# Kernel optimization log

Measured on AMD Instinct MI355X. Metric: run time of the kernel, lower is better.

## Reference

```python
import jax, jax.numpy as jnp
import numpy as np

TOP_K = 2


def setup_inputs() -> dict:
    key = jax.random.key(0)
    k1, k2, k3, k4, k5 = jax.random.split(key, 5)
    H, F, E = 1024, 2048, 8
    B, S = 2, 1024
    return {
        "hidden_states": jax.random.normal(k1, (B, S, H), dtype=jnp.float32),
        "gate_w": jax.random.normal(k2, (E, H), dtype=jnp.float32) * (1.0 / np.sqrt(H)),
        "w1": jax.random.normal(k3, (E, F, H), dtype=jnp.float32) * (1.0 / np.sqrt(H)),
        "w2": jax.random.normal(k4, (E, H, F), dtype=jnp.float32) * (1.0 / np.sqrt(F)),
        "w3": jax.random.normal(k5, (E, F, H), dtype=jnp.float32) * (1.0 / np.sqrt(H)),
    }


def reference(hidden_states, gate_w, w1, w2, w3):
    B, S, H = hidden_states.shape
    E = gate_w.shape[0]
    x = hidden_states.reshape(-1, H)  # [T, H]

    # Router: softmax in float32, top-k, renormalize (exact Mixtral math)
    router_logits = x @ gate_w.T  # [T, E]
    probs = jax.nn.softmax(router_logits.astype(jnp.float32), axis=-1)
    routing_weights, selected = jax.lax.top_k(probs, TOP_K)  # [T, K]
    routing_weights = routing_weights / routing_weights.sum(axis=-1, keepdims=True)
    routing_weights = routing_weights.astype(x.dtype)

    # Per-token combine weight for each expert: [T, E]
    combine = (jax.nn.one_hot(selected, E, dtype=x.dtype) * routing_weights[..., None]).sum(axis=1)

    # Dense grouped expert SwiGLU MLP (zero combine weight for unselected experts
    # makes this strictly equivalent to the gathered/dispatched computation)
    h = jnp.einsum('th,efh->etf', x, w1)   # [E, T, F]
    g = jnp.einsum('th,efh->etf', x, w3)   # [E, T, F]
    mid = jax.nn.silu(h) * g               # SwiGLU
    expert_out = jnp.einsum('etf,ehf->eth', mid, w2)  # [E, T, H]
    out = jnp.einsum('eth,te->th', expert_out, combine)  # weighted combine

    return out.reshape(B, S, H), router_logits
```

## Files before the change

kernel.cpp:

```cpp
#include <hip/hip_runtime.h>
#include <hip/hip_bf16.h>
#include <math.h>

#define H 1024
#define FF 2048
#define E 8
#define T 2048
#define NSLOT (2*T)
#define SLOT_PAD 128

#define WCONV_BLKS 12288
#define XCONV_BLKS 512
#define ROUTER_BLKS T
#define K1_BLKS (WCONV_BLKS + XCONV_BLKS + ROUTER_BLKS)

typedef __attribute__((ext_vector_type(8))) short s16x8;
typedef __attribute__((ext_vector_type(4))) float f32x4;
typedef __attribute__((ext_vector_type(4))) unsigned int u32x4;

static __device__ __forceinline__ unsigned short f2bf(float f) {
    union { float f; unsigned u; } v; v.f = f;
    unsigned r = v.u + 0x7fff + ((v.u >> 16) & 1);
    return (unsigned short)(r >> 16);
}
static __device__ __forceinline__ float bf2f(unsigned short s) {
    union { unsigned u; float f; } v; v.u = ((unsigned)s) << 16;
    return v.f;
}
static __device__ __forceinline__ unsigned pack2(float a, float b) {
    return (unsigned)f2bf(a) | ((unsigned)f2bf(b) << 16);
}

typedef __attribute__((address_space(3))) unsigned int lds_uint;
typedef const __attribute__((address_space(1))) unsigned int glob_uint;
static __device__ __forceinline__ void gl_lds16(const void* g, void* l) {
    __builtin_amdgcn_global_load_lds((glob_uint*)g, (lds_uint*)l, 16, 0, 0);
}

static __device__ __forceinline__ void expert_range(const int* __restrict__ counts,
                                                    int e, int& off, int& cnt) {
    int acc = 0;
    #pragma unroll
    for (int i = 0; i < E; ++i) {
        int c = counts[i];
        if (i < e) acc += c;
        if (i == e) cnt = c;
    }
    off = acc;
}

__global__ __launch_bounds__(256) void prep_kernel(
    const float* __restrict__ x, const float* __restrict__ gw,
    const float* __restrict__ w1, const float* __restrict__ w3,
    const float* __restrict__ w2,
    unsigned short* __restrict__ w1b, unsigned short* __restrict__ w3b,
    unsigned short* __restrict__ w2b, unsigned short* __restrict__ xb,
    float* __restrict__ logits_out, int* __restrict__ top_id,
    float* __restrict__ top_w, int* __restrict__ counts)
{
    int b = blockIdx.x;
    int tid = threadIdx.x;
    if (b < WCONV_BLKS + XCONV_BLKS) {
        const float* s; unsigned short* d; size_t base;
        if (b < WCONV_BLKS) {
            int r = b >> 12;
            s = (r == 0) ? w1 : (r == 1) ? w3 : w2;
            d = (r == 0) ? w1b : (r == 1) ? w3b : w2b;
            base = (size_t)(b & 4095) * 4096;
        } else {
            s = x; d = xb;
            base = (size_t)(b - WCONV_BLKS) * 4096;
        }
        size_t i0 = base + (size_t)(0 * 256 + tid) * 4;
        size_t i1 = base + (size_t)(1 * 256 + tid) * 4;
        size_t i2 = base + (size_t)(2 * 256 + tid) * 4;
        size_t i3 = base + (size_t)(3 * 256 + tid) * 4;
        f32x4 a0 = __builtin_nontemporal_load((const f32x4*)(s + i0));
        f32x4 a1 = __builtin_nontemporal_load((const f32x4*)(s + i1));
        f32x4 a2 = __builtin_nontemporal_load((const f32x4*)(s + i2));
        f32x4 a3 = __builtin_nontemporal_load((const f32x4*)(s + i3));
        uint2 r0, r1, r2, r3;
        r0.x = pack2(a0.x, a0.y); r0.y = pack2(a0.z, a0.w);
        r1.x = pack2(a1.x, a1.y); r1.y = pack2(a1.z, a1.w);
        r2.x = pack2(a2.x, a2.y); r2.y = pack2(a2.z, a2.w);
        r3.x = pack2(a3.x, a3.y); r3.y = pack2(a3.z, a3.w);
        *(uint2*)(d + i0) = r0;
        *(uint2*)(d + i1) = r1;
        *(uint2*)(d + i2) = r2;
        *(uint2*)(d + i3) = r3;
        return;
    }
    int t = b - (WCONV_BLKS + XCONV_BLKS);
    int e = tid >> 5;
    int l32 = tid & 31;
    const float* xr = x + (size_t)t * H;
    const float* gr = gw + (size_t)e * H;
    float s = 0.f;
    for (int h = l32; h < H; h += 32) s += xr[h] * gr[h];
    for (int off = 16; off; off >>= 1) s += __shfl_down(s, off, 32);
    __shared__ float lg[E];
    if (l32 == 0) lg[e] = s;
    __syncthreads();
    if (tid < E) logits_out[(size_t)t * E + tid] = lg[tid];
    if (tid == 0) {
        int i1 = 0; float b1 = lg[0];
        for (int i = 1; i < E; ++i) if (lg[i] > b1) { b1 = lg[i]; i1 = i; }
        int i2 = -1; float b2 = -INFINITY;
        for (int i = 0; i < E; ++i) if (i != i1 && lg[i] > b2) { b2 = lg[i]; i2 = i; }
        float p2 = expf(b2 - b1);
        float inv = 1.f / (1.f + p2);
        top_id[2*t]   = i1;  top_id[2*t+1] = i2;
        top_w[2*t]    = inv; top_w[2*t+1]  = p2 * inv;
        atomicAdd(&counts[i1], 1);
        atomicAdd(&counts[i2], 1);
    }
}

__global__ __launch_bounds__(256) void assign_kernel(
    const int* __restrict__ top_id, const int* __restrict__ counts,
    int* __restrict__ cursors, int* __restrict__ top_pos,
    int* __restrict__ slot_token)
{
    int t = blockIdx.x * 256 + threadIdx.x;
    if (t >= T) return;
    int offs[E];
    {
        int acc = 0;
        #pragma unroll
        for (int i = 0; i < E; ++i) { offs[i] = acc; acc += counts[i]; }
    }
    #pragma unroll
    for (int k = 0; k < 2; ++k) {
        int e = top_id[2*t + k];
        int p = offs[e] + atomicAdd(&cursors[e], 1);
        top_pos[2*t + k] = p;
        slot_token[p] = t;
    }
}

__global__ __launch_bounds__(256) void gemm1_kernel(
    const unsigned short* __restrict__ xb, const int* __restrict__ slot_token,
    const unsigned short* __restrict__ w1b, const unsigned short* __restrict__ w3b,
    const int* __restrict__ counts, unsigned short* __restrict__ mid)
{
    int e = blockIdx.z;
    int off, cnt;
    expert_range(counts, e, off, cnt);
    int m0 = blockIdx.y * 128;
    if (m0 >= cnt) return;
    int f0 = blockIdx.x * 64;

    __shared__ __align__(16) unsigned short sx[128 * 64];
    __shared__ __align__(16) unsigned short s1[64 * 64];
    __shared__ __align__(16) unsigned short s3[64 * 64];

    int tid = threadIdx.x;
    int wv = tid >> 6, ln = tid & 63;
    int quad = ln >> 4, l16 = ln & 15;
    int wm = wv & 1, wn = wv >> 1;
    int xor7 = l16 & 7;

    const unsigned short* xsrc[4]; unsigned short* xdst[4];
    #pragma unroll
    for (int j = 0; j < 4; ++j) {
        int row = wv * 32 + j * 8 + (ln >> 3);
        int slot = off + m0 + row;
        if (m0 + row >= cnt) slot = off;
        int tok = slot_token[slot];
        int cl = (ln & 7) ^ (row & 7);
        xsrc[j] = xb + (size_t)tok * H + cl * 8;
        xdst[j] = &sx[(wv * 32 + j * 8) * 64];
    }
    const unsigned short *w1s[2], *w3s[2]; unsigned short *d1[2], *d3[2];
    #pragma unroll
    for (int j = 0; j < 2; ++j) {
        int row = wv * 16 + j * 8 + (ln >> 3);
        int cl = (ln & 7) ^ (row & 7);
        w1s[j] = w1b + ((size_t)e * FF + f0 + row) * H + cl * 8;
        w3s[j] = w3b + ((size_t)e * FF + f0 + row) * H + cl * 8;
        d1[j] = &s1[(wv * 16 + j * 8) * 64];
        d3[j] = &s3[(wv * 16 + j * 8) * 64];
    }

    f32x4 acc1[4][2], acc3[4][2];
    #pragma unroll
    for (int i = 0; i < 4; ++i)
        #pragma unroll
        for (int j = 0; j < 2; ++j) {
            acc1[i][j] = (f32x4){0.f, 0.f, 0.f, 0.f};
            acc3[i][j] = (f32x4){0.f, 0.f, 0.f, 0.f};
        }

    for (int k0 = 0; k0 < H; k0 += 64) {
        #pragma unroll
        for (int j = 0; j < 4; ++j) gl_lds16(xsrc[j] + k0, xdst[j]);
        #pragma unroll
        for (int j = 0; j < 2; ++j) { gl_lds16(w1s[j] + k0, d1[j]); gl_lds16(w3s[j] + k0, d3[j]); }
        __syncthreads();
        #pragma unroll
        for (int ks = 0; ks < 2; ++ks) {
            int cph = ((quad + 4 * ks) ^ xor7) << 3;
            s16x8 a[4], b1v[2], b3v[2];
            #pragma unroll
            for (int i = 0; i < 4; ++i)
                a[i] = *(const s16x8*)&sx[(wm * 64 + i * 16 + l16) * 64 + cph];
            #pragma unroll
            for (int j = 0; j < 2; ++j) {
                b1v[j] = *(const s16x8*)&s1[(wn * 32 + j * 16 + l16) * 64 + cph];
                b3v[j] = *(const s16x8*)&s3[(wn * 32 + j * 16 + l16) * 64 + cph];
            }
            #pragma unroll
            for (int i = 0; i < 4; ++i)
                #pragma unroll
                for (int j = 0; j < 2; ++j) {
                    acc1[i][j] = __builtin_amdgcn_mfma_f32_16x16x32_bf16(a[i], b1v[j], acc1[i][j], 0, 0, 0);
                    acc3[i][j] = __builtin_amdgcn_mfma_f32_16x16x32_bf16(a[i], b3v[j], acc3[i][j], 0, 0, 0);
                }
        }
        __syncthreads();
    }

    #pragma unroll
    for (int i = 0; i < 4; ++i) {
        #pragma unroll
        for (int r = 0; r < 4; ++r) {
            int row = wm * 64 + i * 16 + quad * 4 + r;
            if (m0 + row < cnt) {
                size_t base = (size_t)(off + m0 + row) * FF + f0 + wn * 32;
                #pragma unroll
                for (int j = 0; j < 2; ++j) {
                    float h = acc1[i][j][r];
                    float g = acc3[i][j][r];
                    float v = h / (1.f + __expf(-h)) * g;
                    mid[base + j * 16 + l16] = f2bf(v);
                }
            }
        }
    }
}

__global__ __launch_bounds__(256) void gemm2_kernel(
    const unsigned short* __restrict__ mid, const unsigned short* __restrict__ w2b,
    const int* __restrict__ counts, unsigned short* __restrict__ y)
{
    int e = blockIdx.z;
    int off, cnt;
    expert_range(counts, e, off, cnt);
    int m0 = blockIdx.y * 128;
    if (m0 >= cnt) return;
    int n0 = blockIdx.x * 64;

    __shared__ __align__(16) unsigned short sa[128 * 64];
    __shared__ __align__(16) unsigned short sb[64 * 64];

    int tid = threadIdx.x;
    int wv = tid >> 6, ln = tid & 63;
    int quad = ln >> 4, l16 = ln & 15;
    int wm = wv & 1, wn = wv >> 1;
    int xor7 = l16 & 7;

    const unsigned short* asrc[4]; unsigned short* adst[4];
    #pragma unroll
    for (int j = 0; j < 4; ++j) {
        int row = wv * 32 + j * 8 + (ln >> 3);
        int cl = (ln & 7) ^ (row & 7);
        asrc[j] = mid + (size_t)(off + m0 + row) * FF + cl * 8;
        adst[j] = &sa[(wv * 32 + j * 8) * 64];
    }
    const unsigned short* bsrc[2]; unsigned short* bdst[2];
    #pragma unroll
    for (int j = 0; j < 2; ++j) {
        int row = wv * 16 + j * 8 + (ln >> 3);
        int cl = (ln & 7) ^ (row & 7);
        bsrc[j] = w2b + ((size_t)e * H + n0 + row) * FF + cl * 8;
        bdst[j] = &sb[(wv * 16 + j * 8) * 64];
    }

    f32x4 acc[4][2];
    #pragma unroll
    for (int i = 0; i < 4; ++i)
        #pragma unroll
        for (int j = 0; j < 2; ++j) acc[i][j] = (f32x4){0.f, 0.f, 0.f, 0.f};

    for (int k0 = 0; k0 < FF; k0 += 64) {
        #pragma unroll
        for (int j = 0; j < 4; ++j) gl_lds16(asrc[j] + k0, adst[j]);
        #pragma unroll
        for (int j = 0; j < 2; ++j) gl_lds16(bsrc[j] + k0, bdst[j]);
        __syncthreads();
        #pragma unroll
        for (int ks = 0; ks < 2; ++ks) {
            int cph = ((quad + 4 * ks) ^ xor7) << 3;
            s16x8 a[4], b[2];
            #pragma unroll
            for (int i = 0; i < 4; ++i)
                a[i] = *(const s16x8*)&sa[(wm * 64 + i * 16 + l16) * 64 + cph];
            #pragma unroll
            for (int j = 0; j < 2; ++j)
                b[j] = *(const s16x8*)&sb[(wn * 32 + j * 16 + l16) * 64 + cph];
            #pragma unroll
            for (int i = 0; i < 4; ++i)
                #pragma unroll
                for (int j = 0; j < 2; ++j)
                    acc[i][j] = __builtin_amdgcn_mfma_f32_16x16x32_bf16(a[i], b[j], acc[i][j], 0, 0, 0);
        }
        __syncthreads();
    }

    #pragma unroll
    for (int i = 0; i < 4; ++i) {
        #pragma unroll
        for (int r = 0; r < 4; ++r) {
            int row = wm * 64 + i * 16 + quad * 4 + r;
            if (m0 + row < cnt) {
                size_t base = (size_t)(off + m0 + row) * H + n0 + wn * 32;
                #pragma unroll
                for (int j = 0; j < 2; ++j)
                    y[base + j * 16 + l16] = f2bf(acc[i][j][r]);
            }
        }
    }
}

__global__ __launch_bounds__(256) void combine_kernel(
    const unsigned short* __restrict__ y, const int* __restrict__ top_pos,
    const float* __restrict__ top_w, float* __restrict__ out)
{
    int t = blockIdx.x, tid = threadIdx.x;
    int p0 = top_pos[2*t], p1 = top_pos[2*t+1];
    float w0 = top_w[2*t], w1 = top_w[2*t+1];
    ushort4 a = ((const ushort4*)(y + (size_t)p0 * H))[tid];
    ushort4 b = ((const ushort4*)(y + (size_t)p1 * H))[tid];
    float4 o;
    o.x = w0 * bf2f(a.x) + w1 * bf2f(b.x);
    o.y = w0 * bf2f(a.y) + w1 * bf2f(b.y);
    o.z = w0 * bf2f(a.z) + w1 * bf2f(b.z);
    o.w = w0 * bf2f(a.w) + w1 * bf2f(b.w);
    ((float4*)(out + (size_t)t * H))[tid] = o;
}

extern "C" void kernel_launch(void* const* d_in, const int* in_sizes, int n_in,
                              void* d_out, int out_size, void* d_ws, size_t ws_size,
                              hipStream_t stream) {
    const float* x  = (const float*)d_in[0];
    const float* gw = (const float*)d_in[1];
    const float* w1 = (const float*)d_in[2];
    const float* w2 = (const float*)d_in[3];
    const float* w3 = (const float*)d_in[4];
    float* out    = (float*)d_out;
    float* logits = out + (size_t)T * H;

    int* counts      = (int*)d_ws;
    int* cursors     = counts + 8;
    int* top_id      = counts + 16;
    int* top_pos     = top_id + 2*T;
    int* slot_token  = top_pos + 2*T;
    float* top_w     = (float*)(slot_token + NSLOT);
    unsigned short* xb  = (unsigned short*)(top_w + 2*T);
    unsigned short* mid = xb  + (size_t)T * H;
    unsigned short* y   = mid + (size_t)(NSLOT + SLOT_PAD) * FF;
    unsigned short* w1b = y   + (size_t)NSLOT * H;
    unsigned short* w3b = w1b + (size_t)E * FF * H;
    unsigned short* w2b = w3b + (size_t)E * FF * H;

    (void)hipMemsetAsync(counts, 0, 16 * sizeof(int), stream);

    prep_kernel<<<K1_BLKS, 256, 0, stream>>>(x, gw, w1, w3, w2,
                                             w1b, w3b, w2b, xb,
                                             logits, top_id, top_w, counts);
    assign_kernel<<<(T + 255) / 256, 256, 0, stream>>>(top_id, counts, cursors,
                                                       top_pos, slot_token);
    gemm1_kernel<<<dim3(FF / 64, 16, E), 256, 0, stream>>>(xb, slot_token,
                                                           w1b, w3b, counts, mid);
    gemm2_kernel<<<dim3(H / 64, 16, E), 256, 0, stream>>>(mid, w2b, counts, y);
    combine_kernel<<<T, 256, 0, stream>>>(y, top_pos, top_w, out);
}
```

Measured before the change: 396.8 us.

## Fuse fp32-to-bf16 weight conversion into the expert GEMM tile loads

Drops the separate pass that converted all expert weights (w1, w3, w2) to bf16 in the prep kernel. The GEMM kernels now read fp32 weights directly, pack them to bf16 in registers and write them to swizzled LDS, replacing the async global-to-LDS copies for the weight tiles. This avoids writing and re-reading about 100 MB of bf16 weights per call. In exchange, each weight tile is loaded and converted several times (once per token-tile block), reading twice the bytes per tile, and the loads now go through registers with synchronous LDS stores.

```diff
diff --git a/kernel.cpp b/kernel.cpp
--- a/kernel.cpp
+++ b/kernel.cpp
@@ -9,10 +9,9 @@
 #define NSLOT (2*T)
 #define SLOT_PAD 128
 
-#define WCONV_BLKS 12288
 #define XCONV_BLKS 512
 #define ROUTER_BLKS T
-#define K1_BLKS (WCONV_BLKS + XCONV_BLKS + ROUTER_BLKS)
+#define K1_BLKS (XCONV_BLKS + ROUTER_BLKS)
 
 typedef __attribute__((ext_vector_type(8))) short s16x8;
 typedef __attribute__((ext_vector_type(4))) float f32x4;
@@ -49,48 +48,43 @@
     off = acc;
 }
 
+static __device__ __forceinline__ u32x4 pack8(f32x4 a, f32x4 b) {
+    u32x4 r;
+    r.x = pack2(a.x, a.y); r.y = pack2(a.z, a.w);
+    r.z = pack2(b.x, b.y); r.w = pack2(b.z, b.w);
+    return r;
+}
+
 __global__ __launch_bounds__(256) void prep_kernel(
     const float* __restrict__ x, const float* __restrict__ gw,
-    const float* __restrict__ w1, const float* __restrict__ w3,
-    const float* __restrict__ w2,
-    unsigned short* __restrict__ w1b, unsigned short* __restrict__ w3b,
-    unsigned short* __restrict__ w2b, unsigned short* __restrict__ xb,
+    unsigned short* __restrict__ xb,
     float* __restrict__ logits_out, int* __restrict__ top_id,
     float* __restrict__ top_w, int* __restrict__ counts)
 {
     int b = blockIdx.x;
     int tid = threadIdx.x;
-    if (b < WCONV_BLKS + XCONV_BLKS) {
-        const float* s; unsigned short* d; size_t base;
-        if (b < WCONV_BLKS) {
-            int r = b >> 12;
-            s = (r == 0) ? w1 : (r == 1) ? w3 : w2;
-            d = (r == 0) ? w1b : (r == 1) ? w3b : w2b;
-            base = (size_t)(b & 4095) * 4096;
-        } else {
-            s = x; d = xb;
-            base = (size_t)(b - WCONV_BLKS) * 4096;
-        }
+    if (b < XCONV_BLKS) {
+        size_t base = (size_t)b * 4096;
         size_t i0 = base + (size_t)(0 * 256 + tid) * 4;
         size_t i1 = base + (size_t)(1 * 256 + tid) * 4;
         size_t i2 = base + (size_t)(2 * 256 + tid) * 4;
         size_t i3 = base + (size_t)(3 * 256 + tid) * 4;
-        f32x4 a0 = __builtin_nontemporal_load((const f32x4*)(s + i0));
-        f32x4 a1 = __builtin_nontemporal_load((const f32x4*)(s + i1));
-        f32x4 a2 = __builtin_nontemporal_load((const f32x4*)(s + i2));
-        f32x4 a3 = __builtin_nontemporal_load((const f32x4*)(s + i3));
+        f32x4 a0 = *(const f32x4*)(x + i0);
+        f32x4 a1 = *(const f32x4*)(x + i1);
+        f32x4 a2 = *(const f32x4*)(x + i2);
+        f32x4 a3 = *(const f32x4*)(x + i3);
         uint2 r0, r1, r2, r3;
         r0.x = pack2(a0.x, a0.y); r0.y = pack2(a0.z, a0.w);
         r1.x = pack2(a1.x, a1.y); r1.y = pack2(a1.z, a1.w);
         r2.x = pack2(a2.x, a2.y); r2.y = pack2(a2.z, a2.w);
         r3.x = pack2(a3.x, a3.y); r3.y = pack2(a3.z, a3.w);
-        *(uint2*)(d + i0) = r0;
-        *(uint2*)(d + i1) = r1;
-        *(uint2*)(d + i2) = r2;
-        *(uint2*)(d + i3) = r3;
+        *(uint2*)(xb + i0) = r0;
+        *(uint2*)(xb + i1) = r1;
+        *(uint2*)(xb + i2) = r2;
+        *(uint2*)(xb + i3) = r3;
         return;
     }
-    int t = b - (WCONV_BLKS + XCONV_BLKS);
+    int t = b - XCONV_BLKS;
     int e = tid >> 5;
     int l32 = tid & 31;
     const float* xr = x + (size_t)t * H;
@@ -140,7 +134,7 @@
 
 __global__ __launch_bounds__(256) void gemm1_kernel(
     const unsigned short* __restrict__ xb, const int* __restrict__ slot_token,
-    const unsigned short* __restrict__ w1b, const unsigned short* __restrict__ w3b,
+    const float* __restrict__ w1f, const float* __restrict__ w3f,
     const int* __restrict__ counts, unsigned short* __restrict__ mid)
 {
     int e = blockIdx.z;
@@ -171,15 +165,15 @@
         xsrc[j] = xb + (size_t)tok * H + cl * 8;
         xdst[j] = &sx[(wv * 32 + j * 8) * 64];
     }
-    const unsigned short *w1s[2], *w3s[2]; unsigned short *d1[2], *d3[2];
-    #pragma unroll
-    for (int j = 0; j < 2; ++j) {
-        int row = wv * 16 + j * 8 + (ln >> 3);
-        int cl = (ln & 7) ^ (row & 7);
-        w1s[j] = w1b + ((size_t)e * FF + f0 + row) * H + cl * 8;
-        w3s[j] = w3b + ((size_t)e * FF + f0 + row) * H + cl * 8;
-        d1[j] = &s1[(wv * 16 + j * 8) * 64];
-        d3[j] = &s3[(wv * 16 + j * 8) * 64];
+    const float* w1s[2]; const float* w3s[2]; int bdst[2];
+    #pragma unroll
+    for (int h = 0; h < 2; ++h) {
+        int slot = h * 256 + tid;
+        int row = slot >> 3;
+        int g = slot & 7;
+        w1s[h] = w1f + ((size_t)e * FF + f0 + row) * H + g * 8;
+        w3s[h] = w3f + ((size_t)e * FF + f0 + row) * H + g * 8;
+        bdst[h] = row * 64 + ((g ^ (row & 7)) << 3);
     }
 
     f32x4 acc1[4][2], acc3[4][2];
@@ -195,7 +189,14 @@
         #pragma unroll
         for (int j = 0; j < 4; ++j) gl_lds16(xsrc[j] + k0, xdst[j]);
         #pragma unroll
-        for (int j = 0; j < 2; ++j) { gl_lds16(w1s[j] + k0, d1[j]); gl_lds16(w3s[j] + k0, d3[j]); }
+        for (int h = 0; h < 2; ++h) {
+            f32x4 u0 = *(const f32x4*)(w1s[h] + k0);
+            f32x4 u1 = *(const f32x4*)(w1s[h] + k0 + 4);
+            f32x4 v0 = *(const f32x4*)(w3s[h] + k0);
+            f32x4 v1 = *(const f32x4*)(w3s[h] + k0 + 4);
+            *(u32x4*)&s1[bdst[h]] = pack8(u0, u1);
+            *(u32x4*)&s3[bdst[h]] = pack8(v0, v1);
+        }
         __syncthreads();
         #pragma unroll
         for (int ks = 0; ks < 2; ++ks) {
@@ -240,7 +241,7 @@
 }
 
 __global__ __launch_bounds__(256) void gemm2_kernel(
-    const unsigned short* __restrict__ mid, const unsigned short* __restrict__ w2b,
+    const unsigned short* __restrict__ mid, const float* __restrict__ w2f,
     const int* __restrict__ counts, unsigned short* __restrict__ y)
 {
     int e = blockIdx.z;
@@ -267,13 +268,14 @@
         asrc[j] = mid + (size_t)(off + m0 + row) * FF + cl * 8;
         adst[j] = &sa[(wv * 32 + j * 8) * 64];
     }
-    const unsigned short* bsrc[2]; unsigned short* bdst[2];
-    #pragma unroll
-    for (int j = 0; j < 2; ++j) {
-        int row = wv * 16 + j * 8 + (ln >> 3);
-        int cl = (ln & 7) ^ (row & 7);
-        bsrc[j] = w2b + ((size_t)e * H + n0 + row) * FF + cl * 8;
-        bdst[j] = &sb[(wv * 16 + j * 8) * 64];
+    const float* w2s[2]; int bdst[2];
+    #pragma unroll
+    for (int h = 0; h < 2; ++h) {
+        int slot = h * 256 + tid;
+        int row = slot >> 3;
+        int g = slot & 7;
+        w2s[h] = w2f + ((size_t)e * H + n0 + row) * FF + g * 8;
+        bdst[h] = row * 64 + ((g ^ (row & 7)) << 3);
     }
 
     f32x4 acc[4][2];
@@ -286,7 +288,11 @@
         #pragma unroll
         for (int j = 0; j < 4; ++j) gl_lds16(asrc[j] + k0, adst[j]);
         #pragma unroll
-        for (int j = 0; j < 2; ++j) gl_lds16(bsrc[j] + k0, bdst[j]);
+        for (int h = 0; h < 2; ++h) {
+            f32x4 u0 = *(const f32x4*)(w2s[h] + k0);
+            f32x4 u1 = *(const f32x4*)(w2s[h] + k0 + 4);
+            *(u32x4*)&sb[bdst[h]] = pack8(u0, u1);
+        }
         __syncthreads();
         #pragma unroll
         for (int ks = 0; ks < 2; ++ks) {
@@ -359,19 +365,15 @@
     unsigned short* xb  = (unsigned short*)(top_w + 2*T);
     unsigned short* mid = xb  + (size_t)T * H;
     unsigned short* y   = mid + (size_t)(NSLOT + SLOT_PAD) * FF;
-    unsigned short* w1b = y   + (size_t)NSLOT * H;
-    unsigned short* w3b = w1b + (size_t)E * FF * H;
-    unsigned short* w2b = w3b + (size_t)E * FF * H;
 
     (void)hipMemsetAsync(counts, 0, 16 * sizeof(int), stream);
 
-    prep_kernel<<<K1_BLKS, 256, 0, stream>>>(x, gw, w1, w3, w2,
-                                             w1b, w3b, w2b, xb,
+    prep_kernel<<<K1_BLKS, 256, 0, stream>>>(x, gw, xb,
                                              logits, top_id, top_w, counts);
     assign_kernel<<<(T + 255) / 256, 256, 0, stream>>>(top_id, counts, cursors,
                                                        top_pos, slot_token);
     gemm1_kernel<<<dim3(FF / 64, 16, E), 256, 0, stream>>>(xb, slot_token,
-                                                           w1b, w3b, counts, mid);
-    gemm2_kernel<<<dim3(H / 64, 16, E), 256, 0, stream>>>(mid, w2b, counts, y);
+                                                           w1, w3, counts, mid);
+    gemm2_kernel<<<dim3(H / 64, 16, E), 256, 0, stream>>>(mid, w2, counts, y);
     combine_kernel<<<T, 256, 0, stream>>>(y, top_pos, top_w, out);
 }
```

Result: slower. 416.6 us (+5.0%).
